# Kernel tuning notes

Measured on AMD Instinct MI355X. Metric: run time of the kernel, lower is better.

The kernel has to match this reference:

```python
import jax, jax.numpy as jnp
import numpy as np

H = 32        # num_attention_heads (query heads)
G = 8         # num_query_groups (KV heads)
D = 128       # head_dim
HID = 4096    # hidden_size
THETA = 10000.0


def _rope(x, pos):
    # x: [B, h, S, D]; pos: [S]. Rotate-half (LLaMA) convention.
    half = D // 2
    inv_freq = 1.0 / (THETA ** (jnp.arange(0, half, dtype=jnp.float32) / half))
    ang = pos[:, None].astype(jnp.float32) * inv_freq[None, :]   # [S, half]
    cos = jnp.cos(ang)[None, None]                               # [1,1,S,half]
    sin = jnp.sin(ang)[None, None]
    x1, x2 = x[..., :half], x[..., half:]
    return jnp.concatenate([x1 * cos - x2 * sin, x1 * sin + x2 * cos], axis=-1)


def setup_inputs() -> dict:
    key = jax.random.key(0)
    ks = jax.random.split(key, 9)
    s = 0.02
    return {
        "hidden_states": jax.random.normal(ks[0], (1, 2048, HID), jnp.float32),
        "Wq": jax.random.normal(ks[1], (HID, H * D), jnp.float32) * s,
        "bq": jnp.zeros((H * D,), jnp.float32),
        "Wk": jax.random.normal(ks[2], (HID, G * D), jnp.float32) * s,
        "bk": jnp.zeros((G * D,), jnp.float32),
        "Wv": jax.random.normal(ks[3], (HID, G * D), jnp.float32) * s,
        "bv": jnp.zeros((G * D,), jnp.float32),
        "Wo": jax.random.normal(ks[4], (H * D, HID), jnp.float32) * s,
        "bo": jnp.zeros((HID,), jnp.float32),
    }


def reference(hidden_states, Wq, bq, Wk, bk, Wv, bv, Wo, bo):
    B, S, _ = hidden_states.shape
    R = H // G  # query heads per KV group

    q = hidden_states @ Wq + bq  # [B,S,H*D]
    k = hidden_states @ Wk + bk  # [B,S,G*D]
    v = hidden_states @ Wv + bv  # [B,S,G*D]

    q = q.reshape(B, S, H, D).transpose(0, 2, 1, 3)  # [B,H,S,D]
    k = k.reshape(B, S, G, D).transpose(0, 2, 1, 3)  # [B,G,S,D]
    v = v.reshape(B, S, G, D).transpose(0, 2, 1, 3)  # [B,G,S,D]

    pos = jnp.arange(S)
    q = _rope(q, pos)
    k = _rope(k, pos)

    # Grouped attention: broadcast KV across the R query heads of each group
    qg = q.reshape(B, G, R, S, D)
    scores = jnp.einsum('bgrsd,bgtd->bgrst', qg, k) / jnp.sqrt(jnp.float32(D))
    causal = jnp.tril(jnp.ones((S, S), dtype=bool))
    scores = jnp.where(causal[None, None, None], scores, jnp.finfo(scores.dtype).min)
    probs = jax.nn.softmax(scores, axis=-1)
    ctx = jnp.einsum('bgrst,bgtd->bgrsd', probs, v)          # [B,G,R,S,D]
    ctx = ctx.reshape(B, H, S, D).transpose(0, 2, 1, 3).reshape(B, S, H * D)
    return ctx @ Wo + bo
```

## Files before the change

kernel.cpp:

```cpp
#include <hip/hip_runtime.h>
#include <hip/hip_bf16.h>
#include <math.h>

#define HID   4096
#define NH    32
#define NG    8
#define DH    128
#define SEQ   2048
#define QKV_N 6144
#define KOFF  4096
#define VOFF  5120

typedef __bf16 bf16x8 __attribute__((ext_vector_type(8)));
typedef float  f32x4  __attribute__((ext_vector_type(4)));
using bf16 = __hip_bfloat16;

#define LOG2E 1.4426950408889634f
#define SCALE 0.08838834764831845f

typedef const __attribute__((address_space(1))) void* gas_p;
typedef __attribute__((address_space(3))) void* las_p;
__device__ __forceinline__ void async_copy16(void* lds, const void* g) {
  __builtin_amdgcn_global_load_lds((gas_p)g, (las_p)lds, 16, 0, 0);
}

__device__ __forceinline__ unsigned pack2(float a, float b) {
  union { bf16 h[2]; unsigned u; } t;
  t.h[0] = __float2bfloat16(a);
  t.h[1] = __float2bfloat16(b);
  return t.u;
}

__global__ __launch_bounds__(256) void prepass_kernel(const float* __restrict__ X,
                                                      const float* __restrict__ Wq, const float* __restrict__ Wk,
                                                      const float* __restrict__ Wv, const float* __restrict__ Wo,
                                                      const float* __restrict__ bq, const float* __restrict__ bk,
                                                      const float* __restrict__ bv,
                                                      bf16* __restrict__ Xb,
                                                      bf16* __restrict__ Wqkv_t, bf16* __restrict__ Wot,
                                                      float* __restrict__ bqkv) {
  const int bx = blockIdx.x, by = blockIdx.y;
  const int t = threadIdx.x;
  if (bx >= 288) {
    if (by < 24) {
      int i = by * 256 + t;
      if (i < 4096)       bqkv[i] = bq[i];
      else if (i < 5120)  bqkv[i] = bk[i - 4096];
      else                bqkv[i] = bv[i - 5120];
    }
    return;
  }
  if (bx >= 160) {
    int i = ((bx - 160) + 128 * by) * 256 + t;
    float4 v = ((const float4*)X)[i];
    union { bf16 h[4]; uint2 u; } c;
    c.h[0] = __float2bfloat16(v.x);
    c.h[1] = __float2bfloat16(v.y);
    c.h[2] = __float2bfloat16(v.z);
    c.h[3] = __float2bfloat16(v.w);
    ((uint2*)Xb)[i] = c.u;
    return;
  }
  __shared__ bf16 T[64][72];
  const float* W; bf16* dst; int N, ntile;
  if (bx < 64)      { W = Wq; dst = Wqkv_t;                      N = 4096; ntile = bx; }
  else if (bx < 80) { W = Wk; dst = Wqkv_t + (size_t)KOFF * HID; N = 1024; ntile = bx - 64; }
  else if (bx < 96) { W = Wv; dst = Wqkv_t + (size_t)VOFF * HID; N = 1024; ntile = bx - 80; }
  else              { W = Wo; dst = Wot;                         N = 4096; ntile = bx - 96; }
  const int n0 = ntile * 64, k0 = by * 64;
  const int nn = (t & 15) * 4, kk = t >> 4;
#pragma unroll
  for (int p = 0; p < 4; ++p) {
    const int k = kk + p * 16;
    float4 v = *(const float4*)&W[(size_t)(k0 + k) * N + n0 + nn];
    union { bf16 h[4]; uint2 u; } c;
    c.h[0] = __float2bfloat16(v.x);
    c.h[1] = __float2bfloat16(v.y);
    c.h[2] = __float2bfloat16(v.z);
    c.h[3] = __float2bfloat16(v.w);
    *(uint2*)&T[k][nn] = c.u;
  }
  __syncthreads();
  const int kc = t & 7, nr = t >> 3;
#pragma unroll
  for (int p = 0; p < 2; ++p) {
    const int n = nr + p * 32;
    union { bf16 h[8]; uint4 u; } o;
#pragma unroll
    for (int i = 0; i < 8; ++i) o.h[i] = T[kc * 8 + i][n];
    *(uint4*)&dst[(size_t)(n0 + n) * HID + k0 + kc * 8] = o.u;
  }
}

__device__ __forceinline__ void st_out(float* C, size_t idx, float v) { C[idx] = v; }
__device__ __forceinline__ void st_out(bf16*  C, size_t idx, float v) { C[idx] = __float2bfloat16(v); }

template <int BM, typename OutT>
__global__ __launch_bounds__(512, 2) void gemm8_kernel(const bf16* __restrict__ A, const bf16* __restrict__ Bt,
                                                       const float* __restrict__ bias, OutT* __restrict__ C,
                                                       int M, int N, int K) {
  constexpr int MT = BM / 32;
  constexpr int LA = (BM * 32 * 2) / (512 * 16);
  constexpr int LB = 2;

  __shared__ alignas(16) bf16 As[2][2][BM * 32];
  __shared__ alignas(16) bf16 Bs[2][2][256 * 32];

  const int tid = threadIdx.x;
  const int w = tid >> 6, lane = tid & 63, quad = lane >> 4, l16 = lane & 15;
  const int wr = w >> 2, wc = w & 3;
  const int m0 = blockIdx.y * BM, n0 = blockIdx.x * 256;

  const bf16* const Ag = A  + (size_t)m0 * K;
  const bf16* const Bg = Bt + (size_t)n0 * K;

  auto stA = [&](int skt, int db, int kh) {
    const int kb = skt * 64 + kh * 32;
#pragma unroll
    for (int L = 0; L < LA; ++L) {
      const int cib = (L * 8 + w) * 64;
      const int ci  = cib + lane;
      const int r   = ci >> 2;
      const int j   = (ci & 3) ^ ((r >> 1) & 3);
      async_copy16(&As[db][kh][cib * 8], Ag + (size_t)r * K + kb + j * 8);
    }
  };
  auto stB = [&](int skt, int db, int kh) {
    const int kb = skt * 64 + kh * 32;
#pragma unroll
    for (int L = 0; L < LB; ++L) {
      const int cib = (L * 8 + w) * 64;
      const int ci  = cib + lane;
      const int r   = ci >> 2;
      const int j   = (ci & 3) ^ ((r >> 1) & 3);
      async_copy16(&Bs[db][kh][cib * 8], Bg + (size_t)r * K + kb + j * 8);
    }
  };

  auto waitv = [&]() {
    if constexpr (BM == 256) asm volatile("s_waitcnt vmcnt(4)" ::: "memory");
    else                     asm volatile("s_waitcnt vmcnt(3)" ::: "memory");
  };

  bf16x8 af[MT], bf2[2];
  auto ldA = [&](int buf, int kh) {
#pragma unroll
    for (int mf = 0; mf < MT; ++mf) {
      const int r = wr * (BM / 2) + mf * 16 + l16;
      af[mf] = *(const bf16x8*)&As[buf][kh][r * 32 + ((quad ^ ((r >> 1) & 3)) << 3)];
    }
  };
  auto ldB = [&](int buf, int kh, int ph) {
#pragma unroll
    for (int j = 0; j < 2; ++j) {
      const int r = wc * 64 + (ph * 2 + j) * 16 + l16;
      bf2[j] = *(const bf16x8*)&Bs[buf][kh][r * 32 + ((quad ^ ((r >> 1) & 3)) << 3)];
    }
  };

  f32x4 acc[MT][4];
  f32x4 zero4 = {0.f, 0.f, 0.f, 0.f};
#pragma unroll
  for (int mf = 0; mf < MT; ++mf)
#pragma unroll
    for (int nf = 0; nf < 4; ++nf) acc[mf][nf] = zero4;

#define GPHASE(BUF, KH, PH, STAGE_CALL)                                                     \
  do {                                                                                      \
    if (PH == 0) ldA(BUF, KH);                                                              \
    ldB(BUF, KH, PH);                                                                       \
    STAGE_CALL;                                                                             \
    __builtin_amdgcn_s_barrier();                                                           \
    asm volatile("s_waitcnt lgkmcnt(0)" ::: "memory");                                      \
    __builtin_amdgcn_sched_barrier(0);                                                      \
    __builtin_amdgcn_s_setprio(1);                                                          \
    _Pragma("unroll")                                                                       \
    for (int mf = 0; mf < MT; ++mf) {                                                       \
      acc[mf][PH * 2 + 0] =                                                                 \
          __builtin_amdgcn_mfma_f32_16x16x32_bf16(af[mf], bf2[0], acc[mf][PH * 2 + 0], 0, 0, 0); \
      acc[mf][PH * 2 + 1] =                                                                 \
          __builtin_amdgcn_mfma_f32_16x16x32_bf16(af[mf], bf2[1], acc[mf][PH * 2 + 1], 0, 0, 0); \
    }                                                                                       \
    __builtin_amdgcn_s_setprio(0);                                                          \
    waitv();                                                                                \
    __builtin_amdgcn_s_barrier();                                                           \
    asm volatile("" ::: "memory");                                                          \
  } while (0)

  const int KT = K >> 6;

  stA(0, 0, 0); stB(0, 0, 0); stA(0, 0, 1); stB(0, 0, 1);
  waitv();
  __builtin_amdgcn_s_barrier();
  asm volatile("" ::: "memory");

  for (int kt = 0; kt < KT; ++kt) {
    const int buf = kt & 1;
    const int nkt = kt + 1;
    const int skt = nkt < KT ? nkt : KT - 1;
    const int db  = nkt & 1;
    GPHASE(buf, 0, 0, stA(skt, db, 0));
    GPHASE(buf, 0, 1, stB(skt, db, 0));
    GPHASE(buf, 1, 0, stA(skt, db, 1));
    GPHASE(buf, 1, 1, stB(skt, db, 1));
  }
#undef GPHASE

  asm volatile("s_waitcnt vmcnt(0)" ::: "memory");

#pragma unroll
  for (int nf = 0; nf < 4; ++nf) {
    const int col = n0 + wc * 64 + nf * 16 + l16;
    const float bv = bias[col];
#pragma unroll
    for (int mf = 0; mf < MT; ++mf) {
#pragma unroll
      for (int r = 0; r < 4; ++r) {
        const int row = m0 + wr * (BM / 2) + mf * 16 + quad * 4 + r;
        st_out(C, (size_t)row * N + col, acc[mf][nf][r] + bv);
      }
    }
  }
}

__global__ __launch_bounds__(256) void rope_vtrans_kernel(bf16* __restrict__ qkv, bf16* __restrict__ vt) {
  __shared__ bf16 tle[32][33];
  const int bx = blockIdx.x;
  const int tid = threadIdx.x;
  if (bx < 2560) {
    int t = bx * 256 + tid;
    int c  = t & 7;
    int hs = (t >> 3) % 40;
    int s  = t / 320;
    int base = (hs < 32) ? hs * 128 : KOFF + (hs - 32) * 128;
    bf16* p = qkv + (size_t)s * QKV_N + base + c * 8;
    union { bf16x8 v; bf16 h[8]; } a, b, ra, rb;
    a.v = *(bf16x8*)p;
    b.v = *(bf16x8*)(p + 64);
#pragma unroll
    for (int j = 0; j < 8; ++j) {
      int d = c * 8 + j;
      float inv = expf(d * -0.14391156862f);
      float ang = (float)s * inv;
      float sn, cs;
      sincosf(ang, &sn, &cs);
      float x1 = __bfloat162float(a.h[j]);
      float x2 = __bfloat162float(b.h[j]);
      ra.h[j] = __float2bfloat16(x1 * cs - x2 * sn);
      rb.h[j] = __float2bfloat16(x1 * sn + x2 * cs);
    }
    *(bf16x8*)p        = ra.v;
    *(bf16x8*)(p + 64) = rb.v;
  } else {
    const int b = bx - 2560;
    const int s0 = (b & 63) * 32, d0 = ((b >> 6) & 3) * 32, g = b >> 8;
    const int tx = tid & 31, ty = tid >> 5;
#pragma unroll
    for (int i = 0; i < 4; ++i)
      tle[ty + i * 8][tx] = qkv[(size_t)(s0 + ty + i * 8) * QKV_N + VOFF + g * 128 + d0 + tx];
    __syncthreads();
#pragma unroll
    for (int i = 0; i < 4; ++i)
      vt[(size_t)(g * 128 + d0 + ty + i * 8) * SEQ + s0 + tx] = tle[tx][ty + i * 8];
  }
}

__global__ __launch_bounds__(512, 4) void attn_kernel(const bf16* __restrict__ qkv, const bf16* __restrict__ vt,
                                                      bf16* __restrict__ ctx) {
  __shared__ alignas(16) bf16 Ks[2][2][32][128];
  __shared__ alignas(16) bf16 Vs[2][2][64][64];
  __shared__ float rs1[64];
  float* const red = (float*)&Ks[0][0][0][0];

  const int bx = blockIdx.x;
  const int h  = blockIdx.y;
  const int g  = h >> 2;
  const int tid = threadIdx.x;
  const int w = tid >> 6;
  const int gid = w >> 2, wq = w & 3;
  const int lane = tid & 63, quad = lane >> 4, l16 = lane & 15;

  const float c1 = SCALE * LOG2E;
  const float c2 = 12.0f * LOG2E;

  const int addrA = (((quad & 1) << 5) + l16) * 4;
  const int addrB = addrA + 64;
  const bool hiq = quad >= 2;

  f32x4 zero4 = {0.f, 0.f, 0.f, 0.f};

  auto stage = [&](int kt2, int buf) {
    const int ktg = 2 * kt2 + gid;
    const bf16* kg = qkv + (size_t)(ktg * 32) * QKV_N + KOFF + g * 128;
    const bf16* vg = vt + (size_t)(g * 128) * SEQ + ktg * 32;
#pragma unroll
    for (int i = 0; i < 2; ++i) {
      const int c = (i * 4 + wq) * 64 + lane;
      {
        const int key = c >> 4, j = c & 15;
        const int js = (j & 8) | ((j ^ key) & 7);
        async_copy16(&Ks[gid][buf][0][0] + (size_t)(i * 4 + wq) * 512,
                     kg + (size_t)key * QKV_N + js * 8);
      }
      {
        const int row = c >> 3, d = row * 2 + ((c >> 2) & 1), k8s = c & 3;
        const int vjs = (k8s ^ row) & 3;
        async_copy16(&Vs[gid][buf][0][0] + (size_t)(i * 4 + wq) * 512,
                     vg + (size_t)d * SEQ + vjs * 8);
      }
    }
  };

  for (int ph = 0; ph < 2; ++ph) {
    const int qt = ph ? bx : (31 - bx);

    bf16x8 qf[4];
    {
      const bf16* qp = qkv + (size_t)(qt * 64 + wq * 16 + l16) * QKV_N + h * 128 + quad * 8;
#pragma unroll
      for (int ks = 0; ks < 4; ++ks) qf[ks] = *(const bf16x8*)(qp + ks * 32);
    }

    f32x4 o[8];
#pragma unroll
    for (int dt = 0; dt < 8; ++dt) o[dt] = zero4;
    float rsum = 0.f;

    __syncthreads();
    stage(0, 0);

    for (int kt2 = 0; kt2 <= qt; ++kt2) {
      const int cur = kt2 & 1;
      __syncthreads();
      if (kt2 + 1 <= qt) stage(kt2 + 1, 1 - cur);

      f32x4 s[2];
#pragma unroll
      for (int nt = 0; nt < 2; ++nt) {
        s[nt] = zero4;
#pragma unroll
        for (int ks = 0; ks < 4; ++ks) {
          const int ch = ks * 4 + quad;
          bf16x8 kf = *(const bf16x8*)&Ks[gid][cur][nt * 16 + l16][((ch & 8) | ((ch ^ l16) & 7)) * 8];
          s[nt] = __builtin_amdgcn_mfma_f32_16x16x32_bf16(kf, qf[ks], s[nt], 0, 0, 0);
        }
      }

#pragma unroll
      for (int nt = 0; nt < 2; ++nt)
#pragma unroll
        for (int r = 0; r < 4; ++r)
          s[nt][r] = exp2f(fmaf(s[nt][r], c1, -c2));

      if (kt2 == qt) {
        const int koff = gid * 32;
        const int q_local = wq * 16 + l16;
#pragma unroll
        for (int nt = 0; nt < 2; ++nt)
#pragma unroll
          for (int r = 0; r < 4; ++r)
            if (koff + nt * 16 + quad * 4 + r > q_local) s[nt][r] = 0.f;
      }

      rsum += (s[0][0] + s[0][1]) + (s[0][2] + s[0][3]) +
              (s[1][0] + s[1][1]) + (s[1][2] + s[1][3]);

      unsigned pk[2][2];
#pragma unroll
      for (int nt = 0; nt < 2; ++nt) {
        pk[nt][0] = pack2(s[nt][0], s[nt][1]);
        pk[nt][1] = pack2(s[nt][2], s[nt][3]);
      }
      int a0l = __builtin_amdgcn_ds_bpermute(addrA, (int)pk[0][0]);
      int a1l = __builtin_amdgcn_ds_bpermute(addrA, (int)pk[0][1]);
      int b0l = __builtin_amdgcn_ds_bpermute(addrB, (int)pk[0][0]);
      int b1l = __builtin_amdgcn_ds_bpermute(addrB, (int)pk[0][1]);
      int a0h = __builtin_amdgcn_ds_bpermute(addrA, (int)pk[1][0]);
      int a1h = __builtin_amdgcn_ds_bpermute(addrA, (int)pk[1][1]);
      int b0h = __builtin_amdgcn_ds_bpermute(addrB, (int)pk[1][0]);
      int b1h = __builtin_amdgcn_ds_bpermute(addrB, (int)pk[1][1]);
      union { int u[4]; bf16x8 v; } pf;
      pf.u[0] = hiq ? a0h : a0l;
      pf.u[1] = hiq ? a1h : a1l;
      pf.u[2] = hiq ? b0h : b0l;
      pf.u[3] = hiq ? b1h : b1l;

#pragma unroll
      for (int dt = 0; dt < 8; ++dt) {
        const int d = dt * 16 + l16, row = d >> 1;
        const int slot = (quad ^ row) & 3;
        bf16x8 vf = *(const bf16x8*)&Vs[gid][cur][row][(d & 1) * 32 + slot * 8];
        o[dt] = __builtin_amdgcn_mfma_f32_16x16x32_bf16(vf, pf.v, o[dt], 0, 0, 0);
      }
    }

    rsum += __shfl_xor(rsum, 16, 64);
    rsum += __shfl_xor(rsum, 32, 64);

    __syncthreads();
    if (gid == 1) {
#pragma unroll
      for (int dt = 0; dt < 8; ++dt)
        *(f32x4*)&red[(((wq * 8 + dt) * 64) + lane) * 4] = o[dt];
      if (quad == 0) rs1[wq * 16 + l16] = rsum;
    }
    __syncthreads();
    if (gid == 0) {
      const float inv = 1.0f / (rsum + rs1[wq * 16 + l16]);
      const int srow = qt * 64 + wq * 16 + l16;
      bf16* cp = ctx + (size_t)srow * HID + h * 128 + quad * 4;
#pragma unroll
      for (int dt = 0; dt < 8; ++dt) {
        f32x4 sum = o[dt] + *(const f32x4*)&red[(((wq * 8 + dt) * 64) + lane) * 4];
        union { bf16 hh[4]; uint2 u; } ov;
#pragma unroll
        for (int r = 0; r < 4; ++r) ov.hh[r] = __float2bfloat16(sum[r] * inv);
        *(uint2*)(cp + dt * 16) = ov.u;
      }
    }
  }
}

extern "C" void kernel_launch(void* const* d_in, const int* in_sizes, int n_in,
                              void* d_out, int out_size, void* d_ws, size_t ws_size,
                              hipStream_t stream) {
  const float* X  = (const float*)d_in[0];
  const float* Wq = (const float*)d_in[1];
  const float* bq = (const float*)d_in[2];
  const float* Wk = (const float*)d_in[3];
  const float* bk = (const float*)d_in[4];
  const float* Wv = (const float*)d_in[5];
  const float* bv = (const float*)d_in[6];
  const float* Wo = (const float*)d_in[7];
  const float* bo = (const float*)d_in[8];
  float* out = (float*)d_out;

  char* ws = (char*)d_ws;
  size_t off = 0;
  auto alloc = [&](size_t bytes) { char* p = ws + off; off += (bytes + 255) & ~255ULL; return p; };
  bf16*  Xb     = (bf16*) alloc((size_t)SEQ * HID * 2);
  bf16*  Wqkv_t = (bf16*) alloc((size_t)QKV_N * HID * 2);
  bf16*  Wot    = (bf16*) alloc((size_t)HID * HID * 2);
  float* bqkv   = (float*)alloc((size_t)QKV_N * 4);
  bf16*  QKV    = (bf16*) alloc((size_t)SEQ * QKV_N * 2);
  bf16*  Vt     = (bf16*) alloc((size_t)NG * DH * SEQ * 2);
  bf16*  Ctx    = (bf16*) alloc((size_t)SEQ * HID * 2);

  prepass_kernel<<<dim3(289, 64), 256, 0, stream>>>(X, Wq, Wk, Wv, Wo, bq, bk, bv,
                                                    Xb, Wqkv_t, Wot, bqkv);
  gemm8_kernel<256, bf16><<<dim3(QKV_N / 256, SEQ / 256), 512, 0, stream>>>(Xb, Wqkv_t, bqkv, QKV, SEQ, QKV_N, HID);
  rope_vtrans_kernel<<<2560 + 2048, 256, 0, stream>>>(QKV, Vt);
  attn_kernel<<<dim3(16, NH), 512, 0, stream>>>(QKV, Vt, Ctx);
  gemm8_kernel<128, float><<<dim3(HID / 256, SEQ / 128), 512, 0, stream>>>(Ctx, Wot, bo, out, SEQ, HID, HID);
}
```

Before: 501.1 us.

## Switch GEMM to triple-buffered LDS pipeline with k-step of 32

Replaces the double-buffered 64-wide k-tile GEMM pipeline with a three-stage ring of 32-wide k-slices, prefetching two slices ahead. The loads are split into an even phase (A plus half of B) and an odd phase (the other half of B), with vmcnt waits retuned to match. The aim is deeper latency hiding of global-to-LDS copies behind MFMA work. In exchange it issues twice as many barriers per unit of K, and the B row remapping and waitcnt values have to be exactly right for correctness.

```diff
diff --git a/kernel.cpp b/kernel.cpp
--- a/kernel.cpp
+++ b/kernel.cpp
@@ -96,15 +96,14 @@
 __device__ __forceinline__ void st_out(bf16*  C, size_t idx, float v) { C[idx] = __float2bfloat16(v); }
 
 template <int BM, typename OutT>
-__global__ __launch_bounds__(512, 2) void gemm8_kernel(const bf16* __restrict__ A, const bf16* __restrict__ Bt,
+__global__ __launch_bounds__(512, 2) void gemm9_kernel(const bf16* __restrict__ A, const bf16* __restrict__ Bt,
                                                        const float* __restrict__ bias, OutT* __restrict__ C,
                                                        int M, int N, int K) {
-  constexpr int MT = BM / 32;
-  constexpr int LA = (BM * 32 * 2) / (512 * 16);
-  constexpr int LB = 2;
-
-  __shared__ alignas(16) bf16 As[2][2][BM * 32];
-  __shared__ alignas(16) bf16 Bs[2][2][256 * 32];
+  constexpr int MT  = BM / 32;
+  constexpr int LAE = BM / 128;
+
+  __shared__ alignas(16) bf16 As3[3][BM * 32];
+  __shared__ alignas(16) bf16 Bs3[3][256 * 32];
 
   const int tid = threadIdx.x;
   const int w = tid >> 6, lane = tid & 63, quad = lane >> 4, l16 = lane & 15;
@@ -114,47 +113,57 @@
   const bf16* const Ag = A  + (size_t)m0 * K;
   const bf16* const Bg = Bt + (size_t)n0 * K;
 
-  auto stA = [&](int skt, int db, int kh) {
-    const int kb = skt * 64 + kh * 32;
-#pragma unroll
-    for (int L = 0; L < LA; ++L) {
+  auto stage_E = [&](int skt, int db) {
+    const int kb = skt * 32;
+#pragma unroll
+    for (int L = 0; L < LAE; ++L) {
       const int cib = (L * 8 + w) * 64;
       const int ci  = cib + lane;
       const int r   = ci >> 2;
       const int j   = (ci & 3) ^ ((r >> 1) & 3);
-      async_copy16(&As[db][kh][cib * 8], Ag + (size_t)r * K + kb + j * 8);
-    }
-  };
-  auto stB = [&](int skt, int db, int kh) {
-    const int kb = skt * 64 + kh * 32;
-#pragma unroll
-    for (int L = 0; L < LB; ++L) {
-      const int cib = (L * 8 + w) * 64;
-      const int ci  = cib + lane;
-      const int r   = ci >> 2;
-      const int j   = (ci & 3) ^ ((r >> 1) & 3);
-      async_copy16(&Bs[db][kh][cib * 8], Bg + (size_t)r * K + kb + j * 8);
-    }
-  };
-
-  auto waitv = [&]() {
-    if constexpr (BM == 256) asm volatile("s_waitcnt vmcnt(4)" ::: "memory");
-    else                     asm volatile("s_waitcnt vmcnt(3)" ::: "memory");
+      async_copy16(&As3[db][cib * 8], Ag + (size_t)r * K + kb + j * 8);
+    }
+    {
+      const int ci   = w * 64 + lane;
+      const int rloc = ci >> 2;
+      const int r    = ((rloc >> 5) << 6) + (rloc & 31);
+      const int j    = (ci & 3) ^ ((r >> 1) & 3);
+      const int rb   = ((w >> 1) << 6) + ((w & 1) << 4);
+      async_copy16(&Bs3[db][rb * 32], Bg + (size_t)r * K + kb + j * 8);
+    }
+  };
+  auto stage_O = [&](int skt, int db) {
+    const int kb = skt * 32;
+    const int ci   = w * 64 + lane;
+    const int rloc = ci >> 2;
+    const int r    = ((rloc >> 5) << 6) + 32 + (rloc & 31);
+    const int j    = (ci & 3) ^ ((r >> 1) & 3);
+    const int rb   = ((w >> 1) << 6) + 32 + ((w & 1) << 4);
+    async_copy16(&Bs3[db][rb * 32], Bg + (size_t)r * K + kb + j * 8);
+  };
+
+  auto waitE = [&]() {
+    if constexpr (BM == 256) asm volatile("s_waitcnt vmcnt(7)" ::: "memory");
+    else                     asm volatile("s_waitcnt vmcnt(5)" ::: "memory");
+  };
+  auto waitO = [&]() {
+    if constexpr (BM == 256) asm volatile("s_waitcnt vmcnt(5)" ::: "memory");
+    else                     asm volatile("s_waitcnt vmcnt(4)" ::: "memory");
   };
 
   bf16x8 af[MT], bf2[2];
-  auto ldA = [&](int buf, int kh) {
+  auto ldA = [&](int buf) {
 #pragma unroll
     for (int mf = 0; mf < MT; ++mf) {
       const int r = wr * (BM / 2) + mf * 16 + l16;
-      af[mf] = *(const bf16x8*)&As[buf][kh][r * 32 + ((quad ^ ((r >> 1) & 3)) << 3)];
-    }
-  };
-  auto ldB = [&](int buf, int kh, int ph) {
+      af[mf] = *(const bf16x8*)&As3[buf][r * 32 + ((quad ^ ((r >> 1) & 3)) << 3)];
+    }
+  };
+  auto ldB = [&](int buf, int half) {
 #pragma unroll
     for (int j = 0; j < 2; ++j) {
-      const int r = wc * 64 + (ph * 2 + j) * 16 + l16;
-      bf2[j] = *(const bf16x8*)&Bs[buf][kh][r * 32 + ((quad ^ ((r >> 1) & 3)) << 3)];
+      const int r = wc * 64 + (half * 2 + j) * 16 + l16;
+      bf2[j] = *(const bf16x8*)&Bs3[buf][r * 32 + ((quad ^ ((r >> 1) & 3)) << 3)];
     }
   };
 
@@ -165,46 +174,54 @@
 #pragma unroll
     for (int nf = 0; nf < 4; ++nf) acc[mf][nf] = zero4;
 
-#define GPHASE(BUF, KH, PH, STAGE_CALL)                                                     \
-  do {                                                                                      \
-    if (PH == 0) ldA(BUF, KH);                                                              \
-    ldB(BUF, KH, PH);                                                                       \
-    STAGE_CALL;                                                                             \
-    __builtin_amdgcn_s_barrier();                                                           \
-    asm volatile("s_waitcnt lgkmcnt(0)" ::: "memory");                                      \
-    __builtin_amdgcn_sched_barrier(0);                                                      \
-    __builtin_amdgcn_s_setprio(1);                                                          \
-    _Pragma("unroll")                                                                       \
-    for (int mf = 0; mf < MT; ++mf) {                                                       \
-      acc[mf][PH * 2 + 0] =                                                                 \
-          __builtin_amdgcn_mfma_f32_16x16x32_bf16(af[mf], bf2[0], acc[mf][PH * 2 + 0], 0, 0, 0); \
-      acc[mf][PH * 2 + 1] =                                                                 \
-          __builtin_amdgcn_mfma_f32_16x16x32_bf16(af[mf], bf2[1], acc[mf][PH * 2 + 1], 0, 0, 0); \
-    }                                                                                       \
-    __builtin_amdgcn_s_setprio(0);                                                          \
-    waitv();                                                                                \
-    __builtin_amdgcn_s_barrier();                                                           \
-    asm volatile("" ::: "memory");                                                          \
-  } while (0)
-
-  const int KT = K >> 6;
-
-  stA(0, 0, 0); stB(0, 0, 0); stA(0, 0, 1); stB(0, 0, 1);
-  waitv();
+  const int KT = K >> 5;
+
+  stage_E(0, 0); stage_O(0, 0);
+  stage_E(1, 1); stage_O(1, 1);
+  waitO();
   __builtin_amdgcn_s_barrier();
   asm volatile("" ::: "memory");
 
-  for (int kt = 0; kt < KT; ++kt) {
-    const int buf = kt & 1;
-    const int nkt = kt + 1;
-    const int skt = nkt < KT ? nkt : KT - 1;
-    const int db  = nkt & 1;
-    GPHASE(buf, 0, 0, stA(skt, db, 0));
-    GPHASE(buf, 0, 1, stB(skt, db, 0));
-    GPHASE(buf, 1, 0, stA(skt, db, 1));
-    GPHASE(buf, 1, 1, stB(skt, db, 1));
-  }
-#undef GPHASE
+  int buf = 0, db = 2;
+  for (int t = 0; t < KT; ++t) {
+    const int nt2 = t + 2;
+    const int skt = nt2 < KT ? nt2 : KT - 1;
+
+    ldA(buf); ldB(buf, 0);
+    stage_E(skt, db);
+    __builtin_amdgcn_s_barrier();
+    asm volatile("s_waitcnt lgkmcnt(0)" ::: "memory");
+    __builtin_amdgcn_sched_barrier(0);
+    __builtin_amdgcn_s_setprio(1);
+#pragma unroll
+    for (int mf = 0; mf < MT; ++mf) {
+      acc[mf][0] = __builtin_amdgcn_mfma_f32_16x16x32_bf16(af[mf], bf2[0], acc[mf][0], 0, 0, 0);
+      acc[mf][1] = __builtin_amdgcn_mfma_f32_16x16x32_bf16(af[mf], bf2[1], acc[mf][1], 0, 0, 0);
+    }
+    __builtin_amdgcn_s_setprio(0);
+    waitE();
+    __builtin_amdgcn_s_barrier();
+    asm volatile("" ::: "memory");
+
+    ldB(buf, 1);
+    stage_O(skt, db);
+    __builtin_amdgcn_s_barrier();
+    asm volatile("s_waitcnt lgkmcnt(0)" ::: "memory");
+    __builtin_amdgcn_sched_barrier(0);
+    __builtin_amdgcn_s_setprio(1);
+#pragma unroll
+    for (int mf = 0; mf < MT; ++mf) {
+      acc[mf][2] = __builtin_amdgcn_mfma_f32_16x16x32_bf16(af[mf], bf2[0], acc[mf][2], 0, 0, 0);
+      acc[mf][3] = __builtin_amdgcn_mfma_f32_16x16x32_bf16(af[mf], bf2[1], acc[mf][3], 0, 0, 0);
+    }
+    __builtin_amdgcn_s_setprio(0);
+    waitO();
+    __builtin_amdgcn_s_barrier();
+    asm volatile("" ::: "memory");
+
+    buf = (buf == 2) ? 0 : buf + 1;
+    db  = (db  == 2) ? 0 : db  + 1;
+  }
 
   asm volatile("s_waitcnt vmcnt(0)" ::: "memory");
 
@@ -448,8 +465,8 @@
 
   prepass_kernel<<<dim3(289, 64), 256, 0, stream>>>(X, Wq, Wk, Wv, Wo, bq, bk, bv,
                                                     Xb, Wqkv_t, Wot, bqkv);
-  gemm8_kernel<256, bf16><<<dim3(QKV_N / 256, SEQ / 256), 512, 0, stream>>>(Xb, Wqkv_t, bqkv, QKV, SEQ, QKV_N, HID);
+  gemm9_kernel<256, bf16><<<dim3(QKV_N / 256, SEQ / 256), 512, 0, stream>>>(Xb, Wqkv_t, bqkv, QKV, SEQ, QKV_N, HID);
   rope_vtrans_kernel<<<2560 + 2048, 256, 0, stream>>>(QKV, Vt);
   attn_kernel<<<dim3(16, NH), 512, 0, stream>>>(QKV, Vt, Ctx);
-  gemm8_kernel<128, float><<<dim3(HID / 256, SEQ / 128), 512, 0, stream>>>(Ctx, Wot, bo, out, SEQ, HID, HID);
-}
+  gemm9_kernel<128, float><<<dim3(HID / 256, SEQ / 128), 512, 0, stream>>>(Ctx, Wot, bo, out, SEQ, HID, HID);
+}
```

Result: slower. 530.4 us (+5.9%).
